# Kernel optimization log

Measured on AMD Instinct MI355X. Metric: run time of the kernel, lower is better.

## Reference

```python
import jax, jax.numpy as jnp
import numpy as np

HIDDEN = 512
HEADS = 8
HEAD_DIM = HIDDEN // HEADS
THRESH = 0.1
EPS = 1e-8


def setup_inputs() -> dict:
    key = jax.random.key(0)
    ks = jax.random.split(key, 9)
    B, S = 2, 4096
    scale = 1.0 / np.sqrt(HIDDEN)
    x = jax.random.normal(ks[0], (B, S, HIDDEN), dtype=jnp.float32)
    Wq = jax.random.normal(ks[1], (HIDDEN, HIDDEN), dtype=jnp.float32) * scale
    bq = jnp.zeros((HIDDEN,), dtype=jnp.float32)
    Wk = jax.random.normal(ks[2], (HIDDEN, HIDDEN), dtype=jnp.float32) * scale
    bk = jnp.zeros((HIDDEN,), dtype=jnp.float32)
    Wv = jax.random.normal(ks[3], (HIDDEN, HIDDEN), dtype=jnp.float32) * scale
    bv = jnp.zeros((HIDDEN,), dtype=jnp.float32)
    Wo = jax.random.normal(ks[4], (HIDDEN, HIDDEN), dtype=jnp.float32) * scale
    bo = jnp.zeros((HIDDEN,), dtype=jnp.float32)
    return {"x": x, "Wq": Wq, "bq": bq, "Wk": Wk, "bk": bk,
            "Wv": Wv, "bv": bv, "Wo": Wo, "bo": bo}


def reference(x, Wq, bq, Wk, bk, Wv, bv, Wo, bo):
    B, S, _ = x.shape
    # torch Linear: y = x @ W.T + b
    def proj(W, b):
        y = jnp.einsum('bsd,ed->bse', x, W) + b
        return y.reshape(B, S, HEADS, HEAD_DIM).transpose(0, 2, 1, 3)  # [B,H,S,Dh]
    Q = proj(Wq, bq)
    K = proj(Wk, bk)
    V = proj(Wv, bv)
    scores = jnp.einsum('bhqd,bhkd->bhqk', Q, K) / jnp.sqrt(jnp.float32(HEAD_DIM))
    probs = jax.nn.softmax(scores, axis=-1)  # [B,H,S,S]
    probs = jnp.where(probs > THRESH, probs, 0.0)
    probs = probs / (jnp.sum(probs, axis=-1, keepdims=True) + EPS)
    ctx = jnp.einsum('bhqk,bhkd->bhqd', probs, V)
    ctx = ctx.transpose(0, 2, 1, 3).reshape(B, S, HIDDEN)
    return jnp.einsum('bsd,ed->bse', ctx, Wo) + bo
```

## Files before the change

### kernel.cpp

```cpp
#include <hip/hip_runtime.h>

#define S_LEN 4096
#define BATCH 2
#define HID 512
#define HEADS 8
#define HD 64
#define NX (BATCH * S_LEN * HID)
#define WSZ (HID * HID)
#define NBH (BATCH * HEADS)
#define QB 64
#define NBLK (S_LEN / QB * NBH)

typedef short v8s __attribute__((ext_vector_type(8)));
typedef float v4f __attribute__((ext_vector_type(4)));
typedef float v16f __attribute__((ext_vector_type(16)));
typedef unsigned short ushort_t;
typedef const __attribute__((address_space(1))) unsigned gu32;
typedef __attribute__((address_space(3))) unsigned lu32;

__device__ __forceinline__ ushort_t f2bf(float f) {
  unsigned u = __builtin_bit_cast(unsigned, f);
  u += 0x7fffu + ((u >> 16) & 1u);
  return (ushort_t)(u >> 16);
}
__device__ __forceinline__ unsigned pk2(float a, float b) {
  return (__builtin_bit_cast(unsigned, a) >> 16) |
         (__builtin_bit_cast(unsigned, b) & 0xFFFF0000u);
}
__device__ __forceinline__ float fexp2(float x) {
  return __builtin_amdgcn_exp2f(x);
}

__device__ __forceinline__ size_t off16(int s, int d) {
  return (size_t)(s >> 4) * 1024 +
         (size_t)((d >> 5) * 512 + (((s & 15) + 16 * ((d >> 3) & 3)) * 8) + (d & 7));
}

__global__ __launch_bounds__(256) void cvt_k(
    const float* __restrict__ x,
    const float* __restrict__ wq, const float* __restrict__ wk,
    const float* __restrict__ wv, const float* __restrict__ wo,
    ushort_t* __restrict__ dst)
{
  const size_t e = ((size_t)blockIdx.x * 256 + threadIdx.x) * 4;
  const float* src; size_t off;
  if (e < NX) { src = x; off = e; }
  else {
    const size_t we = e - NX;
    const int wi = (int)(we >> 18);
    src = wi == 0 ? wq : wi == 1 ? wk : wi == 2 ? wv : wo;
    off = we & (WSZ - 1);
  }
  float4 v = *(const float4*)&src[off];
  uint2 u; u.x = pk2(v.x, v.y); u.y = pk2(v.z, v.w);
  *(uint2*)&dst[e] = u;
}

__global__ __launch_bounds__(256) void gemm_qkv(
    const ushort_t* __restrict__ X, const ushort_t* __restrict__ Wb,
    const float* __restrict__ bq, const float* __restrict__ bk, const float* __restrict__ bv,
    ushort_t* __restrict__ Qf, ushort_t* __restrict__ Kf, ushort_t* __restrict__ Vw,
    float qscale)
{
  __shared__ ushort_t As[128][32];
  __shared__ ushort_t Bs[128][32];
  const int t = threadIdx.x;
  const int lane = t & 63;
  const int l15 = lane & 15, lg = lane >> 4;
  const int w = t >> 6;
  const int wr = w >> 1, wc = w & 1;
  const int m0 = blockIdx.y * 128;
  const int wsel = blockIdx.x >> 2;
  const int e0 = (blockIdx.x & 3) * 128;
  const ushort_t* W = Wb + (size_t)wsel * WSZ;
  const float* bias = wsel == 0 ? bq : wsel == 1 ? bk : bv;
  const float osc = (wsel == 0) ? qscale : 1.0f;

  v4f acc[4][4] = {};
  const int r0  = t >> 2;
  const int c0  = (t & 3) * 8;
  const int sc0 = (((t & 3) ^ ((t >> 3) & 3))) * 8;
  const int rsw = (l15 >> 1) & 3;

  for (int k0 = 0; k0 < HID; k0 += 32) {
    __syncthreads();
    __builtin_amdgcn_global_load_lds(
        (gu32*)(const void*)&X[(size_t)(m0 + r0) * HID + k0 + sc0],
        (lu32*)(void*)&As[r0][c0], 16, 0, 0);
    __builtin_amdgcn_global_load_lds(
        (gu32*)(const void*)&X[(size_t)(m0 + r0 + 64) * HID + k0 + sc0],
        (lu32*)(void*)&As[r0 + 64][c0], 16, 0, 0);
    __builtin_amdgcn_global_load_lds(
        (gu32*)(const void*)&W[(size_t)(e0 + r0) * HID + k0 + sc0],
        (lu32*)(void*)&Bs[r0][c0], 16, 0, 0);
    __builtin_amdgcn_global_load_lds(
        (gu32*)(const void*)&W[(size_t)(e0 + r0 + 64) * HID + k0 + sc0],
        (lu32*)(void*)&Bs[r0 + 64][c0], 16, 0, 0);
    __syncthreads();
    v8s a[4], b[4];
    #pragma unroll
    for (int fr = 0; fr < 4; ++fr)
      a[fr] = *(const v8s*)&As[wr * 64 + 16 * fr + l15][8 * (lg ^ rsw)];
    #pragma unroll
    for (int fc = 0; fc < 4; ++fc)
      b[fc] = *(const v8s*)&Bs[wc * 64 + 16 * fc + l15][8 * (lg ^ rsw)];
    #pragma unroll
    for (int fr = 0; fr < 4; ++fr)
      #pragma unroll
      for (int fc = 0; fc < 4; ++fc)
        acc[fr][fc] = __builtin_amdgcn_mfma_f32_16x16x32_bf16(a[fr], b[fc], acc[fr][fc], 0, 0, 0);
  }

  #pragma unroll
  for (int fr = 0; fr < 4; ++fr)
    #pragma unroll
    for (int fc = 0; fc < 4; ++fc) {
      const int e = e0 + wc * 64 + 16 * fc + l15;
      const float bval = bias[e];
      #pragma unroll
      for (int r = 0; r < 4; ++r) {
        const int m = m0 + wr * 64 + 16 * fr + 4 * lg + r;
        const float v = (acc[fr][fc][r] + bval) * osc;
        const int bidx = m >> 12, s = m & (S_LEN - 1);
        const int hh = e >> 6, dh = e & 63;
        const size_t hb = ((size_t)(bidx * HEADS + hh)) * (size_t)(S_LEN * HD);
        if (wsel == 2) {
          Vw[hb + (size_t)s * HD + dh] = f2bf(v);
        } else {
          (wsel == 0 ? Qf : Kf)[hb + off16(s, dh)] = f2bf(v);
        }
      }
    }
}

__global__ __launch_bounds__(512, 4) void attn_p1(
    const ushort_t* __restrict__ Qf, const ushort_t* __restrict__ Kf,
    int* __restrict__ Flg)
{
  __shared__ float RedL[4][QB];
  __shared__ float RedM[4][QB];
  __shared__ int bflag;
  const int t = threadIdx.x;
  const int lane = t & 63;
  const int l15 = lane & 15, lg = (lane >> 4) & 3;
  const int w = t >> 6;
  const int rs = w >> 2;
  const int kq = w & 3;
  const int lin = blockIdx.x;
  const int bh = ((lin & 7) << 1) | ((lin >> 3) & 1);
  const int q0 = (lin >> 4) * QB;
  if (t == 0) bflag = 0;

  const size_t hoff = (size_t)bh * (size_t)(S_LEN * HD);
  const ushort_t* Qb = Qf + hoff;
  const ushort_t* Kb = Kf + hoff;

  v8s qa[2][2];
  const int qc0 = (q0 >> 4) + rs * 2;
  #pragma unroll
  for (int tq = 0; tq < 2; ++tq)
    #pragma unroll
    for (int ds = 0; ds < 2; ++ds)
      qa[tq][ds] = *(const v8s*)&Qb[(size_t)(qc0 + tq) * 1024 + ds * 512 + lane * 8];

  float M[2][4], L[2][4];
  #pragma unroll
  for (int tq = 0; tq < 2; ++tq)
    #pragma unroll
    for (int r = 0; r < 4; ++r) { M[tq][r] = -1e30f; L[tq][r] = 0.f; }

  v8s kA[2][2], kB[2][2];

#define LOADK(DST, IDX)                                                     \
  {                                                                         \
    const int kc_ = (kq + 4 * (IDX)) * 2;                                   \
    _Pragma("unroll")                                                       \
    for (int tk = 0; tk < 2; ++tk)                                          \
      _Pragma("unroll")                                                     \
      for (int ds = 0; ds < 2; ++ds)                                        \
        DST[tk][ds] = *(const v8s*)&Kb[(size_t)(kc_ + tk) * 1024 + ds * 512 + lane * 8]; \
  }
#define CHAIN(KX, OUT)                                                      \
  {                                                                         \
    _Pragma("unroll")                                                       \
    for (int tq = 0; tq < 2; ++tq)                                          \
      _Pragma("unroll")                                                     \
      for (int tk = 0; tk < 2; ++tk) {                                      \
        v4f s_ = {0.f, 0.f, 0.f, 0.f};                                      \
        s_ = __builtin_amdgcn_mfma_f32_16x16x32_bf16(qa[tq][0], KX[tk][0], s_, 0, 0, 0); \
        s_ = __builtin_amdgcn_mfma_f32_16x16x32_bf16(qa[tq][1], KX[tk][1], s_, 0, 0, 0); \
        OUT[tq][tk] = s_;                                                   \
      }                                                                     \
  }
#define MERGE(P)                                                            \
  {                                                                         \
    _Pragma("unroll")                                                       \
    for (int tq = 0; tq < 2; ++tq)                                          \
      _Pragma("unroll")                                                     \
      for (int tk = 0; tk < 2; ++tk)                                        \
        _Pragma("unroll")                                                   \
        for (int r = 0; r < 4; ++r) {                                       \
          M[tq][r] = fmaxf(M[tq][r], P[tq][tk][r]);                         \
          L[tq][r] += fexp2(P[tq][tk][r]);                                  \
        }                                                                   \
  }
#define CPY(D, S)                                                           \
  {                                                                         \
    _Pragma("unroll")                                                       \
    for (int tq = 0; tq < 2; ++tq)                                          \
      _Pragma("unroll")                                                     \
      for (int tk = 0; tk < 2; ++tk) D[tq][tk] = S[tq][tk];                 \
  }

  LOADK(kA, 0)
  LOADK(kB, 1)
  v4f prev[2][2], cur[2][2];
  CHAIN(kA, prev)
  for (int i = 1; i < 31; i += 2) {
    LOADK(kA, i + 1)
    CHAIN(kB, cur)
    MERGE(prev)
    CPY(prev, cur)
    LOADK(kB, i + 2)
    CHAIN(kA, cur)
    MERGE(prev)
    CPY(prev, cur)
  }
  CHAIN(kB, cur)
  MERGE(prev)
  MERGE(cur)
#undef LOADK
#undef CHAIN
#undef MERGE
#undef CPY

  #pragma unroll
  for (int tq = 0; tq < 2; ++tq)
    #pragma unroll
    for (int r = 0; r < 4; ++r) {
      float Lv = L[tq][r], Mv = M[tq][r];
      Lv += __shfl_xor(Lv, 1);  Mv = fmaxf(Mv, __shfl_xor(Mv, 1));
      Lv += __shfl_xor(Lv, 2);  Mv = fmaxf(Mv, __shfl_xor(Mv, 2));
      Lv += __shfl_xor(Lv, 4);  Mv = fmaxf(Mv, __shfl_xor(Mv, 4));
      Lv += __shfl_xor(Lv, 8);  Mv = fmaxf(Mv, __shfl_xor(Mv, 8));
      if (l15 == 0) {
        const int row = rs * 32 + tq * 16 + 4 * lg + r;
        RedL[kq][row] = Lv;
        RedM[kq][row] = Mv;
      }
    }
  __syncthreads();
  if (t < QB) {
    const float Lv = RedL[0][t] + RedL[1][t] + RedL[2][t] + RedL[3][t];
    const float Mv = fmaxf(fmaxf(RedM[0][t], RedM[1][t]),
                           fmaxf(RedM[2][t], RedM[3][t]));
    if (Mv >= __log2f(Lv) - 3.3719281f) atomicOr(&bflag, 1);
  }
  __syncthreads();
  if (t == 0) Flg[lin] = bflag;
}

__global__ __launch_bounds__(256) void attn_p2(
    const ushort_t* __restrict__ Qf, const ushort_t* __restrict__ Kf,
    const ushort_t* __restrict__ V, ushort_t* __restrict__ Cb,
    const int* __restrict__ Flg)
{
  const int lin = blockIdx.x;
  if (Flg[lin] == 0) return;
  __shared__ float Osh[QB][HD + 1];
  __shared__ float Dsh[QB];
  __shared__ float RedA[4][QB];
  __shared__ float iLs[QB];
  __shared__ ushort_t Pp[4][32][40];
  __shared__ ushort_t VT[4][HD][40];
  const int t = threadIdx.x;
  const int lane = t & 63;
  const int l31 = lane & 31, hi = lane >> 5;
  const int w = t >> 6;
  const int bh = ((lin & 7) << 1) | ((lin >> 3) & 1);
  const int q0 = (lin >> 4) * QB;
  const size_t hoff = (size_t)bh * (size_t)(S_LEN * HD);
  const ushort_t* Qb = Qf + hoff;
  const ushort_t* Kb = Kf + hoff;
  const ushort_t* Vh = V + hoff;

  if (t < QB) Dsh[t] = 0.f;
  for (int idx = t; idx < QB * HD; idx += 256) Osh[idx >> 6][idx & 63] = 0.f;

#define LD32(DST, BASE, SROW, KS)                                           \
  { ushort_t tmp_[8];                                                       \
    _Pragma("unroll")                                                       \
    for (int j_ = 0; j_ < 8; ++j_)                                          \
      tmp_[j_] = BASE[off16((SROW), (KS) * 16 + 8 * hi + j_)];              \
    DST = *(const v8s*)tmp_; }

  v8s qa[4], qB[4];
  #pragma unroll
  for (int ks = 0; ks < 4; ++ks) {
    LD32(qa[ks], Qb, q0 + l31, ks)
    LD32(qB[ks], Qb, q0 + 32 + l31, ks)
  }

  float L0[16], L1[16];
  #pragma unroll
  for (int j = 0; j < 16; ++j) { L0[j] = 0.f; L1[j] = 0.f; }
  for (int i = 0; i < 32; ++i) {
    const int c = w + 4 * i;
    v8s kb[4];
    #pragma unroll
    for (int ks = 0; ks < 4; ++ks)
      LD32(kb[ks], Kb, c * 32 + l31, ks)
    v16f sa = {}, sb = {};
    #pragma unroll
    for (int ks = 0; ks < 4; ++ks) {
      sa = __builtin_amdgcn_mfma_f32_32x32x16_bf16(qa[ks], kb[ks], sa, 0, 0, 0);
      sb = __builtin_amdgcn_mfma_f32_32x32x16_bf16(qB[ks], kb[ks], sb, 0, 0, 0);
    }
    #pragma unroll
    for (int j = 0; j < 16; ++j) {
      L0[j] += fexp2(sa[j]);
      L1[j] += fexp2(sb[j]);
    }
  }
  #pragma unroll
  for (int rseti = 0; rseti < 2; ++rseti)
    #pragma unroll
    for (int j = 0; j < 16; ++j) {
      float Lv = (rseti == 0) ? L0[j] : L1[j];
      Lv += __shfl_xor(Lv, 1);  Lv += __shfl_xor(Lv, 2);
      Lv += __shfl_xor(Lv, 4);  Lv += __shfl_xor(Lv, 8);
      Lv += __shfl_xor(Lv, 16);
      if (l31 == 0) {
        const int row = rseti * 32 + (j & 3) + 8 * (j >> 2) + 4 * hi;
        RedA[w][row] = Lv;
      }
    }
  __syncthreads();
  if (t < QB)
    iLs[t] = 1.0f / (RedA[0][t] + RedA[1][t] + RedA[2][t] + RedA[3][t]);
  __syncthreads();

  float il[2][16];
  #pragma unroll
  for (int rseti = 0; rseti < 2; ++rseti)
    #pragma unroll
    for (int j = 0; j < 16; ++j)
      il[rseti][j] = iLs[rseti * 32 + (j & 3) + 8 * (j >> 2) + 4 * hi];

  v16f oA[2] = {}, oB[2] = {};
  float den[2][16] = {};

  for (int i = 0; i < 32; ++i) {
    const int c = w + 4 * i;
    v8s kb[4];
    #pragma unroll
    for (int ks = 0; ks < 4; ++ks)
      LD32(kb[ks], Kb, c * 32 + l31, ks)
    v16f sa = {}, sb = {};
    #pragma unroll
    for (int ks = 0; ks < 4; ++ks) {
      sa = __builtin_amdgcn_mfma_f32_32x32x16_bf16(qa[ks], kb[ks], sa, 0, 0, 0);
      sb = __builtin_amdgcn_mfma_f32_32x32x16_bf16(qB[ks], kb[ks], sb, 0, 0, 0);
    }
    {
      const ushort_t* vsrc = &Vh[((size_t)c * 32 + l31) * HD + hi * 32];
      #pragma unroll
      for (int qq = 0; qq < 4; ++qq) {
        uint4 vv = *(const uint4*)&vsrc[qq * 8];
        const ushort_t* pv = (const ushort_t*)&vv;
        #pragma unroll
        for (int jj = 0; jj < 8; ++jj)
          VT[w][hi * 32 + qq * 8 + jj][l31] = pv[jj];
      }
    }
    #pragma unroll
    for (int rseti = 0; rseti < 2; ++rseti) {
      #pragma unroll
      for (int j = 0; j < 16; ++j) {
        const float s = (rseti == 0) ? sa[j] : sb[j];
        const int row = (j & 3) + 8 * (j >> 2) + 4 * hi;
        float p = fexp2(s) * il[rseti][j];
        p = (p > 0.1f) ? p : 0.f;
        den[rseti][j] += p;
        Pp[w][row][l31] = f2bf(p);
      }
      v8s pa0 = *(const v8s*)&Pp[w][l31][8 * hi];
      v8s pa1 = *(const v8s*)&Pp[w][l31][16 + 8 * hi];
      #pragma unroll
      for (int dblk = 0; dblk < 2; ++dblk) {
        v8s vb0 = *(const v8s*)&VT[w][dblk * 32 + l31][8 * hi];
        v8s vb1 = *(const v8s*)&VT[w][dblk * 32 + l31][16 + 8 * hi];
        if (rseti == 0) {
          oA[dblk] = __builtin_amdgcn_mfma_f32_32x32x16_bf16(pa0, vb0, oA[dblk], 0, 0, 0);
          oA[dblk] = __builtin_amdgcn_mfma_f32_32x32x16_bf16(pa1, vb1, oA[dblk], 0, 0, 0);
        } else {
          oB[dblk] = __builtin_amdgcn_mfma_f32_32x32x16_bf16(pa0, vb0, oB[dblk], 0, 0, 0);
          oB[dblk] = __builtin_amdgcn_mfma_f32_32x32x16_bf16(pa1, vb1, oB[dblk], 0, 0, 0);
        }
      }
    }
  }
#undef LD32

  #pragma unroll
  for (int rseti = 0; rseti < 2; ++rseti)
    #pragma unroll
    for (int j = 0; j < 16; ++j) {
      float d = den[rseti][j];
      d += __shfl_xor(d, 1); d += __shfl_xor(d, 2); d += __shfl_xor(d, 4);
      d += __shfl_xor(d, 8); d += __shfl_xor(d, 16);
      const int row = rseti * 32 + (j & 3) + 8 * (j >> 2) + 4 * hi;
      if (l31 == 0) atomicAdd(&Dsh[row], d);
    }
  #pragma unroll
  for (int rseti = 0; rseti < 2; ++rseti)
    #pragma unroll
    for (int dblk = 0; dblk < 2; ++dblk)
      #pragma unroll
      for (int j = 0; j < 16; ++j) {
        const int row = rseti * 32 + (j & 3) + 8 * (j >> 2) + 4 * hi;
        const float val = (rseti == 0) ? oA[dblk][j] : oB[dblk][j];
        atomicAdd(&Osh[row][dblk * 32 + l31], val);
      }
  __syncthreads();
  const int b = bh >> 3, h = bh & 7;
  for (int idx = t; idx < QB * HD; idx += 256) {
    const int row = idx >> 6, d = idx & 63;
    const float val = Osh[row][d] / (Dsh[row] + 1e-8f);
    Cb[((size_t)b * S_LEN + q0 + row) * HID + h * HD + d] = f2bf(val);
  }
}

__global__ __launch_bounds__(256) void gemm_out(
    const ushort_t* __restrict__ X, const ushort_t* __restrict__ W,
    const float* __restrict__ bias, const int* __restrict__ Flg,
    float* __restrict__ Df)
{
  const int t = threadIdx.x;
  const int m0 = blockIdx.y * 64;
  const int e0 = blockIdx.x * 64;

  int fm = 0;
  {
    const int b = m0 >> 12, qblk = (m0 & (S_LEN - 1)) >> 6;
    #pragma unroll
    for (int h = 0; h < HEADS; ++h) {
      const int bhh = b * HEADS + h;
      const int base = (bhh >> 1) | ((bhh & 1) << 3);
      fm |= (Flg[base | (qblk << 4)] ? 1 : 0) << h;
    }
    if (!fm) {
      const int row = t >> 2, c0 = (t & 3) * 16;
      #pragma unroll
      for (int g = 0; g < 4; ++g) {
        const float4 bv = *(const float4*)&bias[e0 + c0 + g * 4];
        *(float4*)&Df[(size_t)(m0 + row) * HID + e0 + c0 + g * 4] = bv;
      }
      return;
    }
  }

  __shared__ ushort_t As[64][40];
  __shared__ ushort_t Bs[64][40];
  const int lane = t & 63;
  const int l15 = lane & 15, lg = lane >> 4;
  const int w = t >> 6;
  const int wr = w >> 1, wc = w & 1;

  v4f acc[2][2] = {};
  const int srow = t >> 2, scol = (t & 3) * 8;
  const uint4 zu = {0u, 0u, 0u, 0u};

  for (int k0 = 0; k0 < HID; k0 += 32) {
    __syncthreads();
    const bool hot = (fm >> (k0 >> 6)) & 1;
    *(uint4*)&As[srow][scol] = hot
        ? *(const uint4*)&X[(size_t)(m0 + srow) * HID + k0 + scol]
        : zu;
    *(uint4*)&Bs[srow][scol] =
        *(const uint4*)&W[(size_t)(e0 + srow) * HID + k0 + scol];
    __syncthreads();
    v8s a[2], b[2];
    #pragma unroll
    for (int fr = 0; fr < 2; ++fr)
      a[fr] = *(const v8s*)&As[wr * 32 + 16 * fr + l15][8 * lg];
    #pragma unroll
    for (int fc = 0; fc < 2; ++fc)
      b[fc] = *(const v8s*)&Bs[wc * 32 + 16 * fc + l15][8 * lg];
    #pragma unroll
    for (int fr = 0; fr < 2; ++fr)
      #pragma unroll
      for (int fc = 0; fc < 2; ++fc)
        acc[fr][fc] = __builtin_amdgcn_mfma_f32_16x16x32_bf16(a[fr], b[fc], acc[fr][fc], 0, 0, 0);
  }

  #pragma unroll
  for (int fr = 0; fr < 2; ++fr)
    #pragma unroll
    for (int fc = 0; fc < 2; ++fc) {
      const int e = e0 + wc * 32 + 16 * fc + l15;
      const float bval = bias[e];
      #pragma unroll
      for (int r = 0; r < 4; ++r) {
        const int m = m0 + wr * 32 + 16 * fr + 4 * lg + r;
        Df[(size_t)m * HID + e] = acc[fr][fc][r] + bval;
      }
    }
}

extern "C" void kernel_launch(void* const* d_in, const int* in_sizes, int n_in,
                              void* d_out, int out_size, void* d_ws, size_t ws_size,
                              hipStream_t stream) {
  const float* x  = (const float*)d_in[0];
  const float* Wq = (const float*)d_in[1];
  const float* bq = (const float*)d_in[2];
  const float* Wk = (const float*)d_in[3];
  const float* bk = (const float*)d_in[4];
  const float* Wv = (const float*)d_in[5];
  const float* bv = (const float*)d_in[6];
  const float* Wo = (const float*)d_in[7];
  const float* bo = (const float*)d_in[8];

  int*      Flg  = (int*)d_ws;
  ushort_t* xb   = (ushort_t*)(Flg + NBLK);
  ushort_t* wqb  = xb + NX;
  ushort_t* wob  = wqb + 3 * WSZ;
  ushort_t* Qf   = wob + WSZ;
  ushort_t* Kf   = Qf + NX;
  ushort_t* Vw   = Kf + NX;
  ushort_t* Cb   = Vw + NX;

  const float qscale = 0.125f * 1.44269504f;

  cvt_k<<<(NX + 4 * WSZ) / 1024, 256, 0, stream>>>(x, Wq, Wk, Wv, Wo, xb);

  gemm_qkv<<<dim3(12, 64), 256, 0, stream>>>(
      xb, wqb, bq, bk, bv, Qf, Kf, Vw, qscale);

  attn_p1<<<NBLK, 512, 0, stream>>>(Qf, Kf, Flg);
  attn_p2<<<NBLK, 256, 0, stream>>>(Qf, Kf, Vw, Cb, Flg);

  gemm_out<<<dim3(8, 128), 256, 0, stream>>>(Cb, wob, bo, Flg, (float*)d_out);
}
```

Baseline: 96.24 us.

## Repartition attn_p1 waves so each covers all 64 query rows over a disjoint key slice

The score-statistics pass now has each of the 8 waves keep all four 16-row query fragments in registers and stream a disjoint interleaved set of 16-key tiles, instead of splitting waves 2x4 over query rows and key quarters. Each K tile is loaded once per block rather than twice, which cuts K global/L2 traffic in half. In exchange each wave holds more Q fragments and accumulators, raising register pressure, and the cross-wave reduction now sums 8 partials instead of 4.

```diff
diff --git a/kernel.cpp b/kernel.cpp
--- a/kernel.cpp
+++ b/kernel.cpp
@@ -137,15 +137,13 @@
     const ushort_t* __restrict__ Qf, const ushort_t* __restrict__ Kf,
     int* __restrict__ Flg)
 {
-  __shared__ float RedL[4][QB];
-  __shared__ float RedM[4][QB];
+  __shared__ float RedL[8][QB];
+  __shared__ float RedM[8][QB];
   __shared__ int bflag;
   const int t = threadIdx.x;
   const int lane = t & 63;
   const int l15 = lane & 15, lg = (lane >> 4) & 3;
   const int w = t >> 6;
-  const int rs = w >> 2;
-  const int kq = w & 3;
   const int lin = blockIdx.x;
   const int bh = ((lin & 7) << 1) | ((lin >> 3) & 1);
   const int q0 = (lin >> 4) * QB;
@@ -155,66 +153,57 @@
   const ushort_t* Qb = Qf + hoff;
   const ushort_t* Kb = Kf + hoff;
 
-  v8s qa[2][2];
-  const int qc0 = (q0 >> 4) + rs * 2;
-  #pragma unroll
-  for (int tq = 0; tq < 2; ++tq)
+  v8s qa[4][2];
+  const int qc0 = q0 >> 4;
+  #pragma unroll
+  for (int tq = 0; tq < 4; ++tq)
     #pragma unroll
     for (int ds = 0; ds < 2; ++ds)
       qa[tq][ds] = *(const v8s*)&Qb[(size_t)(qc0 + tq) * 1024 + ds * 512 + lane * 8];
 
-  float M[2][4], L[2][4];
-  #pragma unroll
-  for (int tq = 0; tq < 2; ++tq)
+  float M[4][4], L[4][4];
+  #pragma unroll
+  for (int tq = 0; tq < 4; ++tq)
     #pragma unroll
     for (int r = 0; r < 4; ++r) { M[tq][r] = -1e30f; L[tq][r] = 0.f; }
 
-  v8s kA[2][2], kB[2][2];
+  v8s kA[2], kB[2];
 
 #define LOADK(DST, IDX)                                                     \
   {                                                                         \
-    const int kc_ = (kq + 4 * (IDX)) * 2;                                   \
-    _Pragma("unroll")                                                       \
-    for (int tk = 0; tk < 2; ++tk)                                          \
-      _Pragma("unroll")                                                     \
-      for (int ds = 0; ds < 2; ++ds)                                        \
-        DST[tk][ds] = *(const v8s*)&Kb[(size_t)(kc_ + tk) * 1024 + ds * 512 + lane * 8]; \
+    const size_t kt_ = (size_t)(w + 8 * (IDX)) * 1024;                      \
+    DST[0] = *(const v8s*)&Kb[kt_ + lane * 8];                              \
+    DST[1] = *(const v8s*)&Kb[kt_ + 512 + lane * 8];                        \
   }
 #define CHAIN(KX, OUT)                                                      \
   {                                                                         \
     _Pragma("unroll")                                                       \
-    for (int tq = 0; tq < 2; ++tq)                                          \
-      _Pragma("unroll")                                                     \
-      for (int tk = 0; tk < 2; ++tk) {                                      \
-        v4f s_ = {0.f, 0.f, 0.f, 0.f};                                      \
-        s_ = __builtin_amdgcn_mfma_f32_16x16x32_bf16(qa[tq][0], KX[tk][0], s_, 0, 0, 0); \
-        s_ = __builtin_amdgcn_mfma_f32_16x16x32_bf16(qa[tq][1], KX[tk][1], s_, 0, 0, 0); \
-        OUT[tq][tk] = s_;                                                   \
-      }                                                                     \
+    for (int tq = 0; tq < 4; ++tq) {                                        \
+      v4f s_ = {0.f, 0.f, 0.f, 0.f};                                        \
+      s_ = __builtin_amdgcn_mfma_f32_16x16x32_bf16(qa[tq][0], KX[0], s_, 0, 0, 0); \
+      s_ = __builtin_amdgcn_mfma_f32_16x16x32_bf16(qa[tq][1], KX[1], s_, 0, 0, 0); \
+      OUT[tq] = s_;                                                         \
+    }                                                                       \
   }
 #define MERGE(P)                                                            \
   {                                                                         \
     _Pragma("unroll")                                                       \
-    for (int tq = 0; tq < 2; ++tq)                                          \
+    for (int tq = 0; tq < 4; ++tq)                                          \
       _Pragma("unroll")                                                     \
-      for (int tk = 0; tk < 2; ++tk)                                        \
-        _Pragma("unroll")                                                   \
-        for (int r = 0; r < 4; ++r) {                                       \
-          M[tq][r] = fmaxf(M[tq][r], P[tq][tk][r]);                         \
-          L[tq][r] += fexp2(P[tq][tk][r]);                                  \
-        }                                                                   \
+      for (int r = 0; r < 4; ++r) {                                         \
+        M[tq][r] = fmaxf(M[tq][r], P[tq][r]);                               \
+        L[tq][r] += fexp2(P[tq][r]);                                        \
+      }                                                                     \
   }
 #define CPY(D, S)                                                           \
   {                                                                         \
     _Pragma("unroll")                                                       \
-    for (int tq = 0; tq < 2; ++tq)                                          \
-      _Pragma("unroll")                                                     \
-      for (int tk = 0; tk < 2; ++tk) D[tq][tk] = S[tq][tk];                 \
+    for (int tq = 0; tq < 4; ++tq) D[tq] = S[tq];                           \
   }
 
   LOADK(kA, 0)
   LOADK(kB, 1)
-  v4f prev[2][2], cur[2][2];
+  v4f prev[4], cur[4];
   CHAIN(kA, prev)
   for (int i = 1; i < 31; i += 2) {
     LOADK(kA, i + 1)
@@ -235,7 +224,7 @@
 #undef CPY
 
   #pragma unroll
-  for (int tq = 0; tq < 2; ++tq)
+  for (int tq = 0; tq < 4; ++tq)
     #pragma unroll
     for (int r = 0; r < 4; ++r) {
       float Lv = L[tq][r], Mv = M[tq][r];
@@ -244,16 +233,19 @@
       Lv += __shfl_xor(Lv, 4);  Mv = fmaxf(Mv, __shfl_xor(Mv, 4));
       Lv += __shfl_xor(Lv, 8);  Mv = fmaxf(Mv, __shfl_xor(Mv, 8));
       if (l15 == 0) {
-        const int row = rs * 32 + tq * 16 + 4 * lg + r;
-        RedL[kq][row] = Lv;
-        RedM[kq][row] = Mv;
+        const int row = tq * 16 + 4 * lg + r;
+        RedL[w][row] = Lv;
+        RedM[w][row] = Mv;
       }
     }
   __syncthreads();
   if (t < QB) {
-    const float Lv = RedL[0][t] + RedL[1][t] + RedL[2][t] + RedL[3][t];
-    const float Mv = fmaxf(fmaxf(RedM[0][t], RedM[1][t]),
-                           fmaxf(RedM[2][t], RedM[3][t]));
+    float Lv = 0.f, Mv = -1e30f;
+    #pragma unroll
+    for (int e8 = 0; e8 < 8; ++e8) {
+      Lv += RedL[e8][t];
+      Mv = fmaxf(Mv, RedM[e8][t]);
+    }
     if (Mv >= __log2f(Lv) - 3.3719281f) atomicOr(&bflag, 1);
   }
   __syncthreads();
```

Result: no change. 96.33 us (+0.1%).
